# Kernel optimization log

Hardware: AMD Instinct MI355X
Metric: run time of the kernel (lower is better)

The kernel has to match this reference:

```python
import math
import jax, jax.numpy as jnp
import numpy as np

POS_DIM = 32


def _fourier_features(pos, dim):
    # pos: [B, M] in [0,1] -> [B, M, dim]
    half = dim // 2
    freqs = jnp.exp(jnp.linspace(0.0, math.log(1000.0), half, dtype=pos.dtype))
    ang = pos[..., None] * freqs                      # [B, M, half]
    out = jnp.concatenate([jnp.sin(ang), jnp.cos(ang)], axis=-1)
    if out.shape[-1] < dim:  # pad if dim is odd (not the case for dim=32)
        pad = jnp.zeros(out.shape[:-1] + (dim - out.shape[-1],), dtype=pos.dtype)
        out = jnp.concatenate([out, pad], axis=-1)
    return out


def setup_inputs() -> dict:
    key = jax.random.key(0)
    k1, k2, k3 = jax.random.split(key, 3)
    B, T, D, M = 8, 8192, 512, 512
    frame_emb = jax.random.normal(k1, (B, T, D), dtype=jnp.float32)
    beat_bounds = jax.random.randint(k2, (B, M, 2), 0, T).astype(jnp.int64)
    # nn.Linear(D + POS_DIM, D): store as [in, out] for x @ W + b
    bound = 1.0 / math.sqrt(D + POS_DIM)
    W = jax.random.uniform(k3, (D + POS_DIM, D), dtype=jnp.float32,
                           minval=-bound, maxval=bound)
    b = jnp.zeros((D,), dtype=jnp.float32)
    return {"frame_emb": frame_emb, "beat_bounds": beat_bounds, "W": W, "b": b}


def reference(frame_emb, beat_bounds, W, b):
    B, T, D = frame_emb.shape
    M = beat_bounds.shape[1]
    dt = frame_emb.dtype

    # clamp bounds exactly as the torch loop does
    s = jnp.clip(beat_bounds[..., 0], 0, T - 1)                 # [B, M]
    e = jnp.maximum(s + 1, jnp.minimum(beat_bounds[..., 1], T))  # [B, M]

    # segment mean via exclusive cumsum: sum(frame_emb[b, s:e]) = cs[e] - cs[s]
    cs = jnp.concatenate(
        [jnp.zeros((B, 1, D), dtype=dt), jnp.cumsum(frame_emb, axis=1)], axis=1
    )  # [B, T+1, D]
    seg_sum = (jnp.take_along_axis(cs, e[..., None], axis=1)
               - jnp.take_along_axis(cs, s[..., None], axis=1))   # [B, M, D]
    counts = (e - s).astype(dt)[..., None]
    out = seg_sum / counts

    # fourier position features over beat index
    pos = (jnp.arange(M, dtype=dt) / max(1, M - 1)).clip(0.0, 1.0)  # [M]
    ff = _fourier_features(jnp.broadcast_to(pos[None, :], (B, M)), POS_DIM)
    out = jnp.concatenate([out, ff], axis=-1) @ W + b               # [B, M, D]
    return out
```

## Files before the change

### kernel.cpp

```cpp
#include <hip/hip_runtime.h>
#include <math.h>

#define B 8
#define T 8192
#define D 512
#define M 512
#define POS 32
#define CHUNK 4
#define NCHUNK (T / CHUNK)
#define GRP 32
#define NGRP (NCHUNK / GRP)
#define BM (B * M)
#define KD 512

typedef __attribute__((ext_vector_type(8))) short short8;
typedef __attribute__((ext_vector_type(4))) short short4v;
typedef __attribute__((ext_vector_type(4))) float floatx4;

static __device__ inline unsigned short f2bf(float f) {
    unsigned int u = __float_as_uint(f);
    unsigned int r = (u + 0x7fffu + ((u >> 16) & 1u)) >> 16;
    return (unsigned short)r;
}
static __device__ inline float bf2f(unsigned short h) {
    return __uint_as_float(((unsigned int)h) << 16);
}

__global__ __launch_bounds__(256) void k_fusedA(const float* __restrict__ fe,
                                                const float* __restrict__ W,
                                                const float* __restrict__ bias,
                                                float* __restrict__ cp,
                                                float* __restrict__ gsum,
                                                short* __restrict__ WhT,
                                                short* __restrict__ WlT,
                                                float* __restrict__ ffout) {
    int blk = blockIdx.x;
    int tid = threadIdx.x;
    if (blk < 512) {
        int b = blk >> 6;
        int g = blk & 63;
        int d2 = tid << 1;
        const float* src = fe + ((size_t)(b * T + g * (GRP * CHUNK)) * D + d2);
        float* cpb = cp + ((size_t)b * NCHUNK + (size_t)g * GRP) * D + d2;
        float2 acc = {0.f, 0.f};
#pragma unroll 4
        for (int c = 0; c < GRP; ++c) {
#pragma unroll
            for (int r = 0; r < CHUNK; ++r) {
                float2 v = *(const float2*)(src + (size_t)(c * CHUNK + r) * D);
                acc.x += v.x; acc.y += v.y;
            }
            *(float2*)(cpb + (size_t)c * D) = acc;
        }
        *(float2*)(gsum + ((size_t)b * NGRP + g) * D + d2) = acc;
    } else if (blk < 640) {
        __shared__ float ws[32][65];
        int wb = blk - 512;
        int k0 = (wb & 15) * 32;
        int n0 = (wb >> 4) * 64;
        {
            int kk = tid >> 3;
            int nn = (tid & 7) << 3;
            const float* src = W + (size_t)(k0 + kk) * D + n0 + nn;
            float4 v0 = *(const float4*)src;
            float4 v1 = *(const float4*)(src + 4);
            ws[kk][nn + 0] = v0.x; ws[kk][nn + 1] = v0.y; ws[kk][nn + 2] = v0.z; ws[kk][nn + 3] = v0.w;
            ws[kk][nn + 4] = v1.x; ws[kk][nn + 5] = v1.y; ws[kk][nn + 6] = v1.z; ws[kk][nn + 7] = v1.w;
        }
        __syncthreads();
        int n = tid >> 2;
        int kq = (tid & 3) << 3;
        short8 hv, lv;
#pragma unroll
        for (int j = 0; j < 8; ++j) {
            float w = ws[kq + j][n];
            unsigned short hb = f2bf(w);
            hv[j] = (short)hb;
            lv[j] = (short)f2bf(w - bf2f(hb));
        }
        size_t off = (size_t)(n0 + n) * KD + k0 + kq;
        *(short8*)(WhT + off) = hv;
        *(short8*)(WlT + off) = lv;
    } else {
        int m = ((blk - 640) << 1) + (tid >> 7);
        int n4 = (tid & 127) << 2;
        float pos = (float)m * (1.0f / 511.0f);
        float4 acc = *(const float4*)(bias + n4);
#pragma unroll
        for (int j = 0; j < 16; ++j) {
            float freq = expf(0.46051701859880914f * (float)j);
            float ang = pos * freq;
            float s = sinf(ang), c = cosf(ang);
            float4 wsn = *(const float4*)(W + (size_t)(D + j) * D + n4);
            float4 wcn = *(const float4*)(W + (size_t)(D + 16 + j) * D + n4);
            acc.x += s * wsn.x + c * wcn.x;
            acc.y += s * wsn.y + c * wcn.y;
            acc.z += s * wsn.z + c * wcn.z;
            acc.w += s * wsn.w + c * wcn.w;
        }
        *(float4*)(ffout + (size_t)m * D + n4) = acc;
    }
}

__global__ __launch_bounds__(256) void k_scan_coarse(const float* __restrict__ gsum,
                                                     float* __restrict__ gx) {
    int b = blockIdx.x;
    int d2 = threadIdx.x << 1;
    float2 acc = {0.f, 0.f};
#pragma unroll
    for (int g = 0; g < NGRP; ++g) {
        *(float2*)(gx + ((size_t)b * (NGRP + 1) + g) * D + d2) = acc;
        float2 v = *(const float2*)(gsum + ((size_t)b * NGRP + g) * D + d2);
        acc.x += v.x; acc.y += v.y;
    }
    *(float2*)(gx + ((size_t)b * (NGRP + 1) + NGRP) * D + d2) = acc;
}

__global__ __launch_bounds__(128) void k_buildx(const float* __restrict__ fe,
                                                const int* __restrict__ bounds,
                                                const float* __restrict__ cp,
                                                const float* __restrict__ gx,
                                                short* __restrict__ Xh,
                                                short* __restrict__ Xl) {
    int bm = blockIdx.x;
    int b = bm / M;
    int b0 = bounds[bm * 2 + 0];
    int b1 = bounds[bm * 2 + 1];
    int s = min(max(b0, 0), T - 1);
    int e = max(min(b1, T), s + 1);
    int cs_ = s >> 2, ce = e >> 2;
    int d4 = threadIdx.x << 2;

    const float* cpb = cp + (size_t)b * NCHUNK * D;
    const float* gxb = gx + (size_t)b * (NGRP + 1) * D;

    float4 acc = *(const float4*)(gxb + (size_t)(ce >> 5) * D + d4);
    if (ce & 31) {
        float4 v = *(const float4*)(cpb + (size_t)(ce - 1) * D + d4);
        acc.x += v.x; acc.y += v.y; acc.z += v.z; acc.w += v.w;
    }
    {
        float4 p = *(const float4*)(gxb + (size_t)(cs_ >> 5) * D + d4);
        acc.x -= p.x; acc.y -= p.y; acc.z -= p.z; acc.w -= p.w;
        if (cs_ & 31) {
            float4 v = *(const float4*)(cpb + (size_t)(cs_ - 1) * D + d4);
            acc.x -= v.x; acc.y -= v.y; acc.z -= v.z; acc.w -= v.w;
        }
    }

    const float* feb = fe + (size_t)b * T * D + d4;
    for (int t = ce * CHUNK; t < e; ++t) {
        float4 v = *(const float4*)(feb + (size_t)t * D);
        acc.x += v.x; acc.y += v.y; acc.z += v.z; acc.w += v.w;
    }
    for (int t = cs_ * CHUNK; t < s; ++t) {
        float4 v = *(const float4*)(feb + (size_t)t * D);
        acc.x -= v.x; acc.y -= v.y; acc.z -= v.z; acc.w -= v.w;
    }
    float inv = 1.0f / (float)(e - s);
    float x0 = acc.x * inv, x1 = acc.y * inv, x2 = acc.z * inv, x3 = acc.w * inv;

    unsigned short h0 = f2bf(x0), h1 = f2bf(x1), h2 = f2bf(x2), h3 = f2bf(x3);
    short4v hv, lv;
    hv[0] = (short)h0; hv[1] = (short)h1; hv[2] = (short)h2; hv[3] = (short)h3;
    lv[0] = (short)f2bf(x0 - bf2f(h0));
    lv[1] = (short)f2bf(x1 - bf2f(h1));
    lv[2] = (short)f2bf(x2 - bf2f(h2));
    lv[3] = (short)f2bf(x3 - bf2f(h3));
    size_t off = (size_t)bm * KD + d4;
    *(short4v*)(Xh + off) = hv;
    *(short4v*)(Xl + off) = lv;
}

__global__ __launch_bounds__(256) void k_gemm(const short* __restrict__ Xh,
                                              const short* __restrict__ Xl,
                                              const short* __restrict__ WhT,
                                              const short* __restrict__ WlT,
                                              const float* __restrict__ ffout,
                                              float* __restrict__ out) {
    __shared__ short Ah[64 * 32], Al[64 * 32], Bh[64 * 32], Bl[64 * 32];
    int n0 = (blockIdx.x & 7) << 6;
    int m0 = (blockIdx.x >> 3) << 6;
    int tid = threadIdx.x;
    int w = tid >> 6;
    int l = tid & 63;
    int lm = l & 15;
    int q = l >> 4;
    int wm = (w & 1) << 5;
    int wn = (w >> 1) << 5;

    floatx4 acc[2][2];
#pragma unroll
    for (int i = 0; i < 2; ++i)
#pragma unroll
        for (int j = 0; j < 2; ++j)
            acc[i][j] = (floatx4){0.f, 0.f, 0.f, 0.f};

    int srow = tid >> 2;
    int skq = tid & 3;
    int sslot = skq ^ ((srow >> 1) & 3);
    int ldsoff = (srow << 5) + (sslot << 3);
    const short* gXh = Xh + (size_t)(m0 + srow) * KD + (skq << 3);
    const short* gXl = Xl + (size_t)(m0 + srow) * KD + (skq << 3);
    const short* gBh = WhT + (size_t)(n0 + srow) * KD + (skq << 3);
    const short* gBl = WlT + (size_t)(n0 + srow) * KD + (skq << 3);

    int aoff[2], boff[2];
#pragma unroll
    for (int mt = 0; mt < 2; ++mt) {
        int row = wm + (mt << 4) + lm;
        aoff[mt] = (row << 5) + ((q ^ ((row >> 1) & 3)) << 3);
    }
#pragma unroll
    for (int nt = 0; nt < 2; ++nt) {
        int row = wn + (nt << 4) + lm;
        boff[nt] = (row << 5) + ((q ^ ((row >> 1) & 3)) << 3);
    }

    for (int k0 = 0; k0 < KD; k0 += 32) {
        short8 vxh = *(const short8*)(gXh + k0);
        short8 vxl = *(const short8*)(gXl + k0);
        short8 vbh = *(const short8*)(gBh + k0);
        short8 vbl = *(const short8*)(gBl + k0);
        __syncthreads();
        *(short8*)(Ah + ldsoff) = vxh;
        *(short8*)(Al + ldsoff) = vxl;
        *(short8*)(Bh + ldsoff) = vbh;
        *(short8*)(Bl + ldsoff) = vbl;
        __syncthreads();

        short8 ah[2], al[2], bh[2], bl[2];
#pragma unroll
        for (int mt = 0; mt < 2; ++mt) {
            ah[mt] = *(const short8*)(Ah + aoff[mt]);
            al[mt] = *(const short8*)(Al + aoff[mt]);
        }
#pragma unroll
        for (int nt = 0; nt < 2; ++nt) {
            bh[nt] = *(const short8*)(Bh + boff[nt]);
            bl[nt] = *(const short8*)(Bl + boff[nt]);
        }
#pragma unroll
        for (int mt = 0; mt < 2; ++mt)
#pragma unroll
            for (int nt = 0; nt < 2; ++nt) {
                acc[mt][nt] = __builtin_amdgcn_mfma_f32_16x16x32_bf16(
                    ah[mt], bh[nt], acc[mt][nt], 0, 0, 0);
                acc[mt][nt] = __builtin_amdgcn_mfma_f32_16x16x32_bf16(
                    ah[mt], bl[nt], acc[mt][nt], 0, 0, 0);
                acc[mt][nt] = __builtin_amdgcn_mfma_f32_16x16x32_bf16(
                    al[mt], bh[nt], acc[mt][nt], 0, 0, 0);
            }
    }

#pragma unroll
    for (int mt = 0; mt < 2; ++mt) {
#pragma unroll
        for (int nt = 0; nt < 2; ++nt) {
            int gcol = n0 + wn + (nt << 4) + lm;
#pragma unroll
            for (int r = 0; r < 4; ++r) {
                int grow = m0 + wm + (mt << 4) + (q << 2) + r;
                float f = ffout[(size_t)(grow & (M - 1)) * D + gcol];
                out[(size_t)grow * D + gcol] = acc[mt][nt][r] + f;
            }
        }
    }
}

extern "C" void kernel_launch(void* const* d_in, const int* in_sizes, int n_in,
                              void* d_out, int out_size, void* d_ws, size_t ws_size,
                              hipStream_t stream) {
    const float* fe = (const float*)d_in[0];
    const int* bounds = (const int*)d_in[1];
    const float* W = (const float*)d_in[2];
    const float* bias = (const float*)d_in[3];
    float* out = (float*)d_out;

    float* cp = (float*)d_ws;
    float* gsum = cp + (size_t)B * NCHUNK * D;
    float* gx = gsum + (size_t)B * NGRP * D;
    float* ffout = gx + (size_t)B * (NGRP + 1) * D;
    short* Xh = (short*)(ffout + (size_t)M * D);
    short* Xl = Xh + (size_t)BM * KD;
    short* WhT = Xl + (size_t)BM * KD;
    short* WlT = WhT + (size_t)KD * D;

    k_fusedA<<<896, 256, 0, stream>>>(fe, W, bias, cp, gsum, WhT, WlT, ffout);
    k_scan_coarse<<<B, 256, 0, stream>>>(gsum, gx);
    k_buildx<<<BM, 128, 0, stream>>>(fe, bounds, cp, gx, Xh, Xl);
    k_gemm<<<64 * 8, 256, 0, stream>>>(Xh, Xl, WhT, WlT, ffout, out);
}
```

Measured before the change: 230.7 us.

## Prefetch next K tile in registers with BK=64 GEMM loop; widen coarse scan grid

The split-bf16 GEMM now processes 64-wide K steps, storing two 32-wide halves in LDS per iteration, and loads the next step's global data into registers before running the MFMAs on the current one. This halves the number of barrier pairs and overlaps global loads with matrix compute, at the cost of more registers and twice the LDS. Separately, the coarse scan is spread over 64 blocks of 64 threads instead of 8 blocks of 256, so more CUs run this serial 64-step chain.

```diff
diff --git a/kernel.cpp b/kernel.cpp
--- a/kernel.cpp
+++ b/kernel.cpp
@@ -102,18 +102,19 @@
     }
 }
 
-__global__ __launch_bounds__(256) void k_scan_coarse(const float* __restrict__ gsum,
-                                                     float* __restrict__ gx) {
-    int b = blockIdx.x;
-    int d2 = threadIdx.x << 1;
-    float2 acc = {0.f, 0.f};
+__global__ __launch_bounds__(64) void k_scan_coarse(const float* __restrict__ gsum,
+                                                    float* __restrict__ gx) {
+    int b = blockIdx.x >> 3;
+    int d = ((blockIdx.x & 7) << 6) + threadIdx.x;
+    const float* gs = gsum + (size_t)b * NGRP * D + d;
+    float* gxp = gx + (size_t)b * (NGRP + 1) * D + d;
+    float acc = 0.f;
 #pragma unroll
     for (int g = 0; g < NGRP; ++g) {
-        *(float2*)(gx + ((size_t)b * (NGRP + 1) + g) * D + d2) = acc;
-        float2 v = *(const float2*)(gsum + ((size_t)b * NGRP + g) * D + d2);
-        acc.x += v.x; acc.y += v.y;
-    }
-    *(float2*)(gx + ((size_t)b * (NGRP + 1) + NGRP) * D + d2) = acc;
+        gxp[(size_t)g * D] = acc;
+        acc += gs[(size_t)g * D];
+    }
+    gxp[(size_t)NGRP * D] = acc;
 }
 
 __global__ __launch_bounds__(128) void k_buildx(const float* __restrict__ fe,
@@ -172,13 +173,15 @@
     *(short4v*)(Xl + off) = lv;
 }
 
+#define BK 64
 __global__ __launch_bounds__(256) void k_gemm(const short* __restrict__ Xh,
                                               const short* __restrict__ Xl,
                                               const short* __restrict__ WhT,
                                               const short* __restrict__ WlT,
                                               const float* __restrict__ ffout,
                                               float* __restrict__ out) {
-    __shared__ short Ah[64 * 32], Al[64 * 32], Bh[64 * 32], Bl[64 * 32];
+    __shared__ short Ah[2][64 * 32], Al[2][64 * 32];
+    __shared__ short Bh[2][64 * 32], Bl[2][64 * 32];
     int n0 = (blockIdx.x & 7) << 6;
     int m0 = (blockIdx.x >> 3) << 6;
     int tid = threadIdx.x;
@@ -217,40 +220,62 @@
         boff[nt] = (row << 5) + ((q ^ ((row >> 1) & 3)) << 3);
     }
 
-    for (int k0 = 0; k0 < KD; k0 += 32) {
-        short8 vxh = *(const short8*)(gXh + k0);
-        short8 vxl = *(const short8*)(gXl + k0);
-        short8 vbh = *(const short8*)(gBh + k0);
-        short8 vbl = *(const short8*)(gBl + k0);
+    short8 pxh[2], pxl[2], pbh[2], pbl[2];
+#pragma unroll
+    for (int h = 0; h < 2; ++h) {
+        pxh[h] = *(const short8*)(gXh + (h << 5));
+        pxl[h] = *(const short8*)(gXl + (h << 5));
+        pbh[h] = *(const short8*)(gBh + (h << 5));
+        pbl[h] = *(const short8*)(gBl + (h << 5));
+    }
+
+    for (int k0 = 0; k0 < KD; k0 += BK) {
         __syncthreads();
-        *(short8*)(Ah + ldsoff) = vxh;
-        *(short8*)(Al + ldsoff) = vxl;
-        *(short8*)(Bh + ldsoff) = vbh;
-        *(short8*)(Bl + ldsoff) = vbl;
+#pragma unroll
+        for (int h = 0; h < 2; ++h) {
+            *(short8*)(&Ah[h][ldsoff]) = pxh[h];
+            *(short8*)(&Al[h][ldsoff]) = pxl[h];
+            *(short8*)(&Bh[h][ldsoff]) = pbh[h];
+            *(short8*)(&Bl[h][ldsoff]) = pbl[h];
+        }
         __syncthreads();
 
-        short8 ah[2], al[2], bh[2], bl[2];
-#pragma unroll
-        for (int mt = 0; mt < 2; ++mt) {
-            ah[mt] = *(const short8*)(Ah + aoff[mt]);
-            al[mt] = *(const short8*)(Al + aoff[mt]);
-        }
-#pragma unroll
-        for (int nt = 0; nt < 2; ++nt) {
-            bh[nt] = *(const short8*)(Bh + boff[nt]);
-            bl[nt] = *(const short8*)(Bl + boff[nt]);
-        }
-#pragma unroll
-        for (int mt = 0; mt < 2; ++mt)
+        int kn = k0 + BK;
+        if (kn < KD) {
+#pragma unroll
+            for (int h = 0; h < 2; ++h) {
+                pxh[h] = *(const short8*)(gXh + kn + (h << 5));
+                pxl[h] = *(const short8*)(gXl + kn + (h << 5));
+                pbh[h] = *(const short8*)(gBh + kn + (h << 5));
+                pbl[h] = *(const short8*)(gBl + kn + (h << 5));
+            }
+        }
+
+#pragma unroll
+        for (int h = 0; h < 2; ++h) {
+            short8 ah[2], al[2], bh[2], bl[2];
+#pragma unroll
+            for (int mt = 0; mt < 2; ++mt) {
+                ah[mt] = *(const short8*)(&Ah[h][aoff[mt]]);
+                al[mt] = *(const short8*)(&Al[h][aoff[mt]]);
+            }
 #pragma unroll
             for (int nt = 0; nt < 2; ++nt) {
-                acc[mt][nt] = __builtin_amdgcn_mfma_f32_16x16x32_bf16(
-                    ah[mt], bh[nt], acc[mt][nt], 0, 0, 0);
-                acc[mt][nt] = __builtin_amdgcn_mfma_f32_16x16x32_bf16(
-                    ah[mt], bl[nt], acc[mt][nt], 0, 0, 0);
-                acc[mt][nt] = __builtin_amdgcn_mfma_f32_16x16x32_bf16(
-                    al[mt], bh[nt], acc[mt][nt], 0, 0, 0);
-            }
+                bh[nt] = *(const short8*)(&Bh[h][boff[nt]]);
+                bl[nt] = *(const short8*)(&Bl[h][boff[nt]]);
+            }
+#pragma unroll
+            for (int mt = 0; mt < 2; ++mt)
+#pragma unroll
+                for (int nt = 0; nt < 2; ++nt) {
+                    acc[mt][nt] = __builtin_amdgcn_mfma_f32_16x16x32_bf16(
+                        ah[mt], bh[nt], acc[mt][nt], 0, 0, 0);
+                    acc[mt][nt] = __builtin_amdgcn_mfma_f32_16x16x32_bf16(
+                        ah[mt], bl[nt], acc[mt][nt], 0, 0, 0);
+                    acc[mt][nt] = __builtin_amdgcn_mfma_f32_16x16x32_bf16(
+                        al[mt], bh[nt], acc[mt][nt], 0, 0, 0);
+                }
+        }
     }
 
 #pragma unroll
@@ -287,7 +312,7 @@
     short* WlT = WhT + (size_t)KD * D;
 
     k_fusedA<<<896, 256, 0, stream>>>(fe, W, bias, cp, gsum, WhT, WlT, ffout);
-    k_scan_coarse<<<B, 256, 0, stream>>>(gsum, gx);
+    k_scan_coarse<<<B * 8, 64, 0, stream>>>(gsum, gx);
     k_buildx<<<BM, 128, 0, stream>>>(fe, bounds, cp, gx, Xh, Xl);
     k_gemm<<<64 * 8, 256, 0, stream>>>(Xh, Xl, WhT, WlT, ffout, out);
 }
```

Result: no change. 227.3 us (-1.5%).
